# Optimization experiments

Hardware: AMD Instinct MI355X
Metric: run time of the kernel (lower is better)

The kernel has to match this reference:

```python
import jax, jax.numpy as jnp
import numpy as np

B, S, H = 4, 2048, 1024
NH, HD = 16, 64
LN_EPS = 1e-5


def _l2norm(x, axis=-1, eps=1e-12):
    n = jnp.sqrt(jnp.sum(x * x, axis=axis, keepdims=True))
    return x / jnp.maximum(n, eps)


def setup_inputs() -> dict:
    key = jax.random.key(0)
    ks = jax.random.split(key, 10)
    sd = 0.02
    x = jax.random.normal(ks[0], (B, S, H), jnp.float32)
    Wq = jax.random.normal(ks[1], (H, H), jnp.float32) * sd
    Wk = jax.random.normal(ks[2], (H, H), jnp.float32) * sd
    Wv = jax.random.normal(ks[3], (H, H), jnp.float32) * sd
    Wa = jax.random.normal(ks[4], (NH, H), jnp.float32) * sd
    ba = jnp.zeros((NH,), jnp.float32)
    Wb = jax.random.normal(ks[5], (NH, H), jnp.float32) * sd
    bb = jnp.zeros((NH,), jnp.float32)
    Wg = jax.random.normal(ks[6], (H, H), jnp.float32) * sd
    Wo = jax.random.normal(ks[7], (H, H), jnp.float32) * sd
    ln_g = jnp.ones((H,), jnp.float32)
    ln_b = jnp.zeros((H,), jnp.float32)
    return {"x": x, "Wq": Wq, "Wk": Wk, "Wv": Wv, "Wa": Wa, "ba": ba,
            "Wb": Wb, "bb": bb, "Wg": Wg, "Wo": Wo, "ln_g": ln_g, "ln_b": ln_b}


def _forward(x, Wq, Wk, Wv, Wa, ba, Wb, bb, Wg, Wo, ln_g, ln_b):
    q = _l2norm((x @ Wq.T).reshape(B, S, NH, HD))  # [B,S,nh,hd]
    k = _l2norm((x @ Wk.T).reshape(B, S, NH, HD))
    v = jax.nn.silu(x @ Wv.T).reshape(B, S, NH, HD)
    alpha = jax.nn.sigmoid(x @ Wa.T + ba)  # [B,S,nh]
    beta = jax.nn.sigmoid(x @ Wb.T + bb)   # [B,S,nh]

    def step(state, inp):
        a_t, b_t, k_t, v_t, q_t = inp  # a,b: [B,nh]; k,v,q: [B,nh,hd]
        a_ = a_t[:, :, None, None]
        b_ = b_t[:, :, None, None]
        kk = k_t[..., :, None] * k_t[..., None, :]  # [B,nh,hd,hd]
        state = a_ * state * (1.0 - b_ * kk) + b_ * (v_t[..., :, None] * k_t[..., None, :])
        out_t = jnp.sum(state * q_t[..., None, :], axis=-1)  # [B,nh,hd]
        return state, out_t

    # time-major xs for scan
    xs = (jnp.moveaxis(alpha, 1, 0), jnp.moveaxis(beta, 1, 0),
          jnp.moveaxis(k, 1, 0), jnp.moveaxis(v, 1, 0), jnp.moveaxis(q, 1, 0))
    state0 = jnp.zeros((B, NH, HD, HD), x.dtype)
    _, outs = jax.lax.scan(step, state0, xs)  # [S,B,nh,hd]
    out = jnp.moveaxis(outs, 0, 1).reshape(B, S, H)

    # LayerNorm over total_dim
    mu = jnp.mean(out, axis=-1, keepdims=True)
    var = jnp.var(out, axis=-1, keepdims=True)
    out = (out - mu) / jnp.sqrt(var + LN_EPS) * ln_g + ln_b

    out = out * jax.nn.silu(x @ Wg.T)
    return out @ Wo.T


def reference(x, Wq, Wk, Wv, Wa, ba, Wb, bb, Wg, Wo, ln_g, ln_b):
    return _forward(x, Wq, Wk, Wv, Wa, ba, Wb, bb, Wg, Wo, ln_g, ln_b)
```

## Files before the change

### kernel.cpp

```cpp
#include <hip/hip_runtime.h>

typedef unsigned short u16;
typedef __bf16 bf16x8 __attribute__((ext_vector_type(8)));
typedef float f32x4 __attribute__((ext_vector_type(4)));

constexpr int Bq  = 4;
constexpr int Sq  = 2048;
constexpr int Hq  = 1024;
constexpr int NHq = 16;
constexpr int HDq = 64;
constexpr int CCH = 16;
constexpr int LCH = 128;

constexpr size_t OFF_WB = 0;
constexpr size_t OFF_XB = 10485760;
constexpr size_t OFF_Q  = 27262976;
constexpr size_t OFF_K  = 60817408;
constexpr size_t OFF_V  = 94371840;
constexpr size_t OFF_G  = 127926272;
constexpr size_t OFF_AL = 161480704;
constexpr size_t OFF_BE = 162004992;
constexpr size_t OFF_P  = 162529280;
constexpr size_t OFF_O  = 179306496;

__device__ __forceinline__ u16 f2bf(float f) {
  unsigned u = __float_as_uint(f);
  u += 0x7fffu + ((u >> 16) & 1u);
  return (u16)(u >> 16);
}
__device__ __forceinline__ float sigmoidf_(float x) { return 1.f / (1.f + __expf(-x)); }

__device__ __forceinline__ void async16(const void* g, void* l) {
  __builtin_amdgcn_global_load_lds((const __attribute__((address_space(1))) void*)g,
                                   (__attribute__((address_space(3))) void*)l, 16, 0, 0);
}

__global__ __launch_bounds__(256) void cvt_x_kernel(const float* __restrict__ in, u16* __restrict__ outp) {
  const size_t i = ((size_t)blockIdx.x * 256 + threadIdx.x) * 4;
  float4 f = *(const float4*)(in + i);
  ushort4 u; u.x = f2bf(f.x); u.y = f2bf(f.y); u.z = f2bf(f.z); u.w = f2bf(f.w);
  *(ushort4*)(outp + i) = u;
}

__global__ __launch_bounds__(256) void cvt_w_kernel(const float* __restrict__ w0, const float* __restrict__ w1,
    const float* __restrict__ w2, const float* __restrict__ w3, const float* __restrict__ w4,
    u16* __restrict__ outp) {
  const int z = blockIdx.z;
  const float* src = (z == 0) ? w0 : (z == 1) ? w1 : (z == 2) ? w2 : (z == 3) ? w3 : w4;
  const size_t i = ((size_t)blockIdx.x * 256 + threadIdx.x) * 4;
  float4 f = *(const float4*)(src + i);
  ushort4 u; u.x = f2bf(f.x); u.y = f2bf(f.y); u.z = f2bf(f.z); u.w = f2bf(f.w);
  *(ushort4*)(outp + (size_t)z * (1024 * 1024) + i) = u;
}

__global__ __launch_bounds__(256) void cvt_ab_kernel(const float* __restrict__ Wa, const float* __restrict__ Wb,
    u16* __restrict__ outp) {
  const size_t i = ((size_t)blockIdx.x * 256 + threadIdx.x) * 4;
  const int row = (int)(i >> 10);
  ushort4 u;
  if (row < 32) {
    const float* src = (row < 16) ? (Wa + i) : (Wb + i - 16 * 1024);
    float4 f = *(const float4*)src;
    u.x = f2bf(f.x); u.y = f2bf(f.y); u.z = f2bf(f.z); u.w = f2bf(f.w);
  } else {
    u.x = u.y = u.z = u.w = 0;
  }
  *(ushort4*)(outp + i) = u;
}

__global__ __launch_bounds__(256) void gemm_bt(const u16* __restrict__ A, const u16* __restrict__ Wall,
    const u16* __restrict__ Wab,
    float* __restrict__ Cq, float* __restrict__ Ck, float* __restrict__ Cv, float* __restrict__ Cg,
    float* __restrict__ al, float* __restrict__ be,
    const float* __restrict__ ba, const float* __restrict__ bb, int mode) {
  constexpr int GK = 1024, GN = 1024;
  const int z = blockIdx.z;
  if (mode == 1 && z == 4 && blockIdx.y > 0) return;
  __shared__ __align__(16) u16 As[128 * 32];
  __shared__ __align__(16) u16 Bs[128 * 32];
  const int tid = threadIdx.x;
  const int w = tid >> 6, lane = tid & 63;
  const int m0 = blockIdx.x * 128, n0 = blockIdx.y * 128;
  const u16* W = (mode == 1 && z == 4) ? Wab : (Wall + (size_t)z * (1024 * 1024));
  const int rrow = lane >> 2;
  const int kc8 = (lane & 3) * 8;
  const u16* gA = A + (size_t)(m0 + w * 32 + rrow) * GK + kc8;
  const u16* gB = W + (size_t)(n0 + w * 32 + rrow) * GK + kc8;
  u16* lA = As + (w * 32) * 32;
  u16* lB = Bs + (w * 32) * 32;
  const int qd = lane >> 4, l15 = lane & 15;
  const int wm = (w >> 1) * 64, wn = (w & 1) * 64;
  f32x4 acc[4][4] = {};
  for (int kt = 0; kt < GK; kt += 32) {
    async16(gA,           lA);
    async16(gA + 16 * GK, lA + 16 * 32);
    async16(gB,           lB);
    async16(gB + 16 * GK, lB + 16 * 32);
    gA += 32; gB += 32;
    __syncthreads();
    bf16x8 af[4], bfr[4];
    #pragma unroll
    for (int i = 0; i < 4; ++i) {
      af[i]  = *(const bf16x8*)(As + (wm + i * 16 + l15) * 32 + qd * 8);
      bfr[i] = *(const bf16x8*)(Bs + (wn + i * 16 + l15) * 32 + qd * 8);
    }
    #pragma unroll
    for (int i = 0; i < 4; ++i)
      #pragma unroll
      for (int j = 0; j < 4; ++j)
        acc[i][j] = __builtin_amdgcn_mfma_f32_16x16x32_bf16(af[i], bfr[j], acc[i][j], 0, 0, 0);
    __syncthreads();
  }
  if (mode == 1 && z == 4) {
    if (wn == 0) {
      const float bav = ba[l15], bbv = bb[l15];
      #pragma unroll
      for (int i = 0; i < 4; ++i) {
        const int row = m0 + wm + i * 16 + qd * 4;
        #pragma unroll
        for (int r = 0; r < 4; ++r) {
          al[(size_t)(row + r) * 16 + l15] = sigmoidf_(acc[i][0][r] + bav);
          be[(size_t)(row + r) * 16 + l15] = sigmoidf_(acc[i][1][r] + bbv);
        }
      }
    }
    return;
  }
  if (mode == 1 && (z == 0 || z == 1)) {
    #pragma unroll
    for (int i = 0; i < 4; ++i)
      #pragma unroll
      for (int r = 0; r < 4; ++r) {
        float ss = acc[i][0][r] * acc[i][0][r] + acc[i][1][r] * acc[i][1][r]
                 + acc[i][2][r] * acc[i][2][r] + acc[i][3][r] * acc[i][3][r];
        ss += __shfl_xor(ss, 1); ss += __shfl_xor(ss, 2);
        ss += __shfl_xor(ss, 4); ss += __shfl_xor(ss, 8);
        const float rn = 1.f / fmaxf(sqrtf(ss), 1e-12f);
        acc[i][0][r] *= rn; acc[i][1][r] *= rn; acc[i][2][r] *= rn; acc[i][3][r] *= rn;
      }
  } else if (mode == 1 && z == 2) {
    #pragma unroll
    for (int i = 0; i < 4; ++i)
      #pragma unroll
      for (int j = 0; j < 4; ++j)
        #pragma unroll
        for (int r = 0; r < 4; ++r)
          acc[i][j][r] = acc[i][j][r] * sigmoidf_(acc[i][j][r]);
  }
  float* C = (mode == 0) ? Cq : ((z == 0) ? Cq : (z == 1) ? Ck : (z == 2) ? Cv : Cg);
  #pragma unroll
  for (int i = 0; i < 4; ++i) {
    const int row = m0 + wm + i * 16 + qd * 4;
    #pragma unroll
    for (int j = 0; j < 4; ++j) {
      const int col = n0 + wn + j * 16 + l15;
      #pragma unroll
      for (int r = 0; r < 4; ++r)
        C[(size_t)(row + r) * GN + col] = acc[i][j][r];
    }
  }
}

struct ScanLds1 { float kb[2][4][16 * 64]; float vb[2][4][16 * 64]; float ab[2][4][32]; };
struct ScanLds2 { float kb[2][4][16 * 64]; float qb[2][4][16 * 64]; float vb[2][4][16 * 64]; float ab[2][4][32]; };

__global__ __launch_bounds__(256) void scan_p1(const float* __restrict__ k, const float* __restrict__ v,
    const float* __restrict__ al, const float* __restrict__ be,
    float* __restrict__ P, float* __restrict__ Q) {
  __shared__ ScanLds1 L;
  const int tid = threadIdx.x, wv = tid >> 6, lane = tid & 63;
  const int bh = blockIdx.x >> 2;
  const int c = (blockIdx.x & 3) * 4 + wv;
  const int b = bh >> 4, h = bh & 15;
  const int r8 = (lane >> 3) * 8, c8 = (lane & 7) * 8;
  const size_t base0 = ((size_t)(b * Sq + c * LCH)) * 1024 + h * 64;
  const size_t ab0   = ((size_t)(b * Sq + c * LCH)) * 16 + h;
  const int tokw = lane >> 4, seg = lane & 15;
  auto stage = [&](int tile, int bi) {
    const size_t tb = base0 + (size_t)tile * 16 * 1024;
    #pragma unroll
    for (int i = 0; i < 4; ++i) {
      async16(k + tb + (size_t)(i * 4 + tokw) * 1024 + seg * 4, &L.kb[bi][wv][i * 256]);
      async16(v + tb + (size_t)(i * 4 + tokw) * 1024 + seg * 4, &L.vb[bi][wv][i * 256]);
    }
    if (lane < 32) {
      const float* src = (lane < 16) ? al : be;
      const int tt = lane & 15;
      L.ab[bi][wv][(lane < 16 ? 0 : 16) + tt] = src[ab0 + (size_t)(tile * 16 + tt) * 16];
    }
  };
  float Pr[64], Qr[64];
  #pragma unroll
  for (int i = 0; i < 64; ++i) { Pr[i] = 1.f; Qr[i] = 0.f; }
  stage(0, 0);
  for (int tile = 0; tile < 8; ++tile) {
    __syncthreads();
    if (tile < 7) stage(tile + 1, (tile + 1) & 1);
    const int bi = tile & 1;
    const float* kbp = L.kb[bi][wv];
    const float* vbp = L.vb[bi][wv];
    const float* abp = L.ab[bi][wv];
    #pragma unroll 2
    for (int tt = 0; tt < 16; ++tt) {
      const float a = abp[tt], bt = abp[16 + tt];
      float4 kcv0 = *(const float4*)(kbp + tt * 64 + c8);
      float4 kcv1 = *(const float4*)(kbp + tt * 64 + c8 + 4);
      float4 krv0 = *(const float4*)(kbp + tt * 64 + r8);
      float4 krv1 = *(const float4*)(kbp + tt * 64 + r8 + 4);
      float4 vrv0 = *(const float4*)(vbp + tt * 64 + r8);
      float4 vrv1 = *(const float4*)(vbp + tt * 64 + r8 + 4);
      const float kcv[8] = {kcv0.x, kcv0.y, kcv0.z, kcv0.w, kcv1.x, kcv1.y, kcv1.z, kcv1.w};
      const float krv[8] = {krv0.x, krv0.y, krv0.z, krv0.w, krv1.x, krv1.y, krv1.z, krv1.w};
      const float vrv[8] = {vrv0.x, vrv0.y, vrv0.z, vrv0.w, vrv1.x, vrv1.y, vrv1.z, vrv1.w};
      const float abt = a * bt;
      float c1[8], c2[8];
      #pragma unroll
      for (int i = 0; i < 8; ++i) { c1[i] = abt * krv[i]; c2[i] = bt * vrv[i]; }
      #pragma unroll
      for (int i = 0; i < 8; ++i)
        #pragma unroll
        for (int j = 0; j < 8; ++j) {
          const int e = i * 8 + j;
          const float A = fmaf(-c1[i], kcv[j], a);
          Qr[e] = fmaf(A, Qr[e], c2[i] * kcv[j]);
          Pr[e] *= A;
        }
    }
  }
  const size_t pbase = ((size_t)bh * CCH + c) * 4096 + (size_t)c8;
  #pragma unroll
  for (int i = 0; i < 8; ++i) {
    const size_t pi = pbase + (size_t)(r8 + i) * 64;
    *(float4*)(P + pi)     = make_float4(Pr[i*8],   Pr[i*8+1], Pr[i*8+2], Pr[i*8+3]);
    *(float4*)(P + pi + 4) = make_float4(Pr[i*8+4], Pr[i*8+5], Pr[i*8+6], Pr[i*8+7]);
    *(float4*)(Q + pi)     = make_float4(Qr[i*8],   Qr[i*8+1], Qr[i*8+2], Qr[i*8+3]);
    *(float4*)(Q + pi + 4) = make_float4(Qr[i*8+4], Qr[i*8+5], Qr[i*8+6], Qr[i*8+7]);
  }
}

__global__ __launch_bounds__(256) void scan_comb(float* __restrict__ P, const float* __restrict__ Q) {
  const int g = blockIdx.x * 256 + threadIdx.x;
  const int elem = g & 4095;
  const int bh = g >> 12;
  float s = 0.f;
  for (int c = 0; c < CCH; ++c) {
    const size_t idx = ((size_t)bh * CCH + c) * 4096 + elem;
    const float p = P[idx], qq = Q[idx];
    P[idx] = s;
    s = fmaf(p, s, qq);
  }
}

__global__ __launch_bounds__(256) void scan_p2(const float* __restrict__ q, const float* __restrict__ k,
    const float* __restrict__ v, const float* __restrict__ al, const float* __restrict__ be,
    const float* __restrict__ Pini, float* __restrict__ o) {
  __shared__ ScanLds2 L;
  const int tid = threadIdx.x, wv = tid >> 6, lane = tid & 63;
  const int bh = blockIdx.x >> 2;
  const int c = (blockIdx.x & 3) * 4 + wv;
  const int b = bh >> 4, h = bh & 15;
  const int cb = lane & 7;
  const int r8 = (lane >> 3) * 8, c8 = cb * 8;
  const size_t base0 = ((size_t)(b * Sq + c * LCH)) * 1024 + h * 64;
  const size_t ab0   = ((size_t)(b * Sq + c * LCH)) * 16 + h;
  const size_t pbase = ((size_t)bh * CCH + c) * 4096 + (size_t)c8;
  const int tokw = lane >> 4, seg = lane & 15;
  auto stage = [&](int tile, int bi) {
    const size_t tb = base0 + (size_t)tile * 16 * 1024;
    #pragma unroll
    for (int i = 0; i < 4; ++i) {
      async16(k + tb + (size_t)(i * 4 + tokw) * 1024 + seg * 4, &L.kb[bi][wv][i * 256]);
      async16(q + tb + (size_t)(i * 4 + tokw) * 1024 + seg * 4, &L.qb[bi][wv][i * 256]);
      async16(v + tb + (size_t)(i * 4 + tokw) * 1024 + seg * 4, &L.vb[bi][wv][i * 256]);
    }
    if (lane < 32) {
      const float* src = (lane < 16) ? al : be;
      const int tt = lane & 15;
      L.ab[bi][wv][(lane < 16 ? 0 : 16) + tt] = src[ab0 + (size_t)(tile * 16 + tt) * 16];
    }
  };
  float st[64];
  #pragma unroll
  for (int i = 0; i < 8; ++i) {
    float4 s0 = *(const float4*)(Pini + pbase + (size_t)(r8 + i) * 64);
    float4 s1 = *(const float4*)(Pini + pbase + (size_t)(r8 + i) * 64 + 4);
    st[i*8]   = s0.x; st[i*8+1] = s0.y; st[i*8+2] = s0.z; st[i*8+3] = s0.w;
    st[i*8+4] = s1.x; st[i*8+5] = s1.y; st[i*8+6] = s1.z; st[i*8+7] = s1.w;
  }
  stage(0, 0);
  const bool hi4 = (cb & 4), hi2 = (cb & 2), hi1 = (cb & 1);
  for (int tile = 0; tile < 8; ++tile) {
    __syncthreads();
    if (tile < 7) stage(tile + 1, (tile + 1) & 1);
    const int bi = tile & 1;
    const float* kbp = L.kb[bi][wv];
    const float* qbp = L.qb[bi][wv];
    const float* vbp = L.vb[bi][wv];
    const float* abp = L.ab[bi][wv];
    #pragma unroll 2
    for (int tt = 0; tt < 16; ++tt) {
      const int t = tile * 16 + tt;
      const float a = abp[tt], bt = abp[16 + tt];
      float4 kcv0 = *(const float4*)(kbp + tt * 64 + c8);
      float4 kcv1 = *(const float4*)(kbp + tt * 64 + c8 + 4);
      float4 qcv0 = *(const float4*)(qbp + tt * 64 + c8);
      float4 qcv1 = *(const float4*)(qbp + tt * 64 + c8 + 4);
      float4 krv0 = *(const float4*)(kbp + tt * 64 + r8);
      float4 krv1 = *(const float4*)(kbp + tt * 64 + r8 + 4);
      float4 vrv0 = *(const float4*)(vbp + tt * 64 + r8);
      float4 vrv1 = *(const float4*)(vbp + tt * 64 + r8 + 4);
      const float kcv[8] = {kcv0.x, kcv0.y, kcv0.z, kcv0.w, kcv1.x, kcv1.y, kcv1.z, kcv1.w};
      const float qcv[8] = {qcv0.x, qcv0.y, qcv0.z, qcv0.w, qcv1.x, qcv1.y, qcv1.z, qcv1.w};
      const float krv[8] = {krv0.x, krv0.y, krv0.z, krv0.w, krv1.x, krv1.y, krv1.z, krv1.w};
      const float vrv[8] = {vrv0.x, vrv0.y, vrv0.z, vrv0.w, vrv1.x, vrv1.y, vrv1.z, vrv1.w};
      const float abt = a * bt;
      float c1[8], c2[8];
      #pragma unroll
      for (int i = 0; i < 8; ++i) { c1[i] = abt * krv[i]; c2[i] = bt * vrv[i]; }
      float p[8];
      #pragma unroll
      for (int i = 0; i < 8; ++i) p[i] = 0.f;
      #pragma unroll
      for (int i = 0; i < 8; ++i)
        #pragma unroll
        for (int j = 0; j < 8; ++j) {
          const int e = i * 8 + j;
          const float A = fmaf(-c1[i], kcv[j], a);
          st[e] = fmaf(A, st[e], c2[i] * kcv[j]);
          p[i] = fmaf(st[e], qcv[j], p[i]);
        }
      float r4[4];
      #pragma unroll
      for (int i = 0; i < 4; ++i) {
        const float send = hi4 ? p[i] : p[i + 4];
        const float recv = __shfl_xor(send, 4);
        r4[i] = (hi4 ? p[i + 4] : p[i]) + recv;
      }
      float r2[2];
      #pragma unroll
      for (int i = 0; i < 2; ++i) {
        const float send = hi2 ? r4[i] : r4[i + 2];
        const float recv = __shfl_xor(send, 2);
        r2[i] = (hi2 ? r4[i + 2] : r4[i]) + recv;
      }
      {
        const float send = hi1 ? r2[0] : r2[1];
        const float recv = __shfl_xor(send, 1);
        const float tot = (hi1 ? r2[1] : r2[0]) + recv;
        o[base0 + (size_t)t * 1024 + lane] = tot;
      }
    }
  }
}

__global__ __launch_bounds__(256) void ln_gate_kernel(const float* __restrict__ o, const float* __restrict__ g,
    const float* __restrict__ ln_g, const float* __restrict__ ln_b, u16* __restrict__ y) {
  const int t = blockIdx.x, tid = threadIdx.x;
  const size_t row = (size_t)t * 1024;
  float4 xv = *(const float4*)(o + row + tid * 4);
  float s  = xv.x + xv.y + xv.z + xv.w;
  float s2 = xv.x * xv.x + xv.y * xv.y + xv.z * xv.z + xv.w * xv.w;
  #pragma unroll
  for (int m = 1; m < 64; m <<= 1) { s += __shfl_xor(s, m); s2 += __shfl_xor(s2, m); }
  __shared__ float red[8];
  const int w = tid >> 6, lane = tid & 63;
  if (lane == 0) { red[w] = s; red[4 + w] = s2; }
  __syncthreads();
  s  = red[0] + red[1] + red[2] + red[3];
  s2 = red[4] + red[5] + red[6] + red[7];
  const float mu = s * (1.f / 1024.f);
  const float var = s2 * (1.f / 1024.f) - mu * mu;
  const float rstd = rsqrtf(var + 1e-5f);
  float4 gv = *(const float4*)(g + row + tid * 4);
  float4 lg = *(const float4*)(ln_g + tid * 4);
  float4 lb = *(const float4*)(ln_b + tid * 4);
  ushort4 u;
  u.x = f2bf(((xv.x - mu) * rstd * lg.x + lb.x) * (gv.x * sigmoidf_(gv.x)));
  u.y = f2bf(((xv.y - mu) * rstd * lg.y + lb.y) * (gv.y * sigmoidf_(gv.y)));
  u.z = f2bf(((xv.z - mu) * rstd * lg.z + lb.z) * (gv.z * sigmoidf_(gv.z)));
  u.w = f2bf(((xv.w - mu) * rstd * lg.w + lb.w) * (gv.w * sigmoidf_(gv.w)));
  *(ushort4*)(y + row + tid * 4) = u;
}

extern "C" void kernel_launch(void* const* d_in, const int* in_sizes, int n_in,
                              void* d_out, int out_size, void* d_ws, size_t ws_size,
                              hipStream_t stream) {
  const float* x    = (const float*)d_in[0];
  const float* Wq   = (const float*)d_in[1];
  const float* Wk   = (const float*)d_in[2];
  const float* Wv   = (const float*)d_in[3];
  const float* Wa   = (const float*)d_in[4];
  const float* ba   = (const float*)d_in[5];
  const float* Wb   = (const float*)d_in[6];
  const float* bb   = (const float*)d_in[7];
  const float* Wg   = (const float*)d_in[8];
  const float* Wo   = (const float*)d_in[9];
  const float* ln_g = (const float*)d_in[10];
  const float* ln_b = (const float*)d_in[11];
  float* out = (float*)d_out;
  char* ws = (char*)d_ws;

  u16*   wb  = (u16*)(ws + OFF_WB);
  u16*   xb  = (u16*)(ws + OFF_XB);
  float* qf  = (float*)(ws + OFF_Q);
  float* kf  = (float*)(ws + OFF_K);
  float* vf  = (float*)(ws + OFF_V);
  float* gf  = (float*)(ws + OFF_G);
  float* al  = (float*)(ws + OFF_AL);
  float* be  = (float*)(ws + OFF_BE);
  u16*   wab = (u16*)(ws + OFF_P);
  float* Pb  = (float*)(ws + OFF_P);
  float* Qc  = (float*)(ws + OFF_XB);
  float* of  = (float*)(ws + OFF_O);
  u16*   yb  = xb;

  cvt_x_kernel<<<8192, 256, 0, stream>>>(x, xb);
  cvt_w_kernel<<<dim3(1024, 1, 5), 256, 0, stream>>>(Wq, Wk, Wv, Wg, Wo, wb);
  cvt_ab_kernel<<<128, 256, 0, stream>>>(Wa, Wb, wab);
  gemm_bt<<<dim3(64, 8, 5), 256, 0, stream>>>(xb, wb, wab, qf, kf, vf, gf, al, be, ba, bb, 1);
  scan_p1<<<256, 256, 0, stream>>>(kf, vf, al, be, Pb, Qc);
  scan_comb<<<1024, 256, 0, stream>>>(Pb, Qc);
  scan_p2<<<256, 256, 0, stream>>>(qf, kf, vf, al, be, Pb, of);
  ln_gate_kernel<<<8192, 256, 0, stream>>>(of, gf, ln_g, ln_b, yb);
  gemm_bt<<<dim3(64, 8, 1), 256, 0, stream>>>(yb, wb + (size_t)4 * 1024 * 1024, wab,
                                              out, out, out, out, al, be, ba, bb, 0);
}
```

Measured before the change: 454.6 us.

## Split each scan chunk's state rows across two waves to double scan parallelism

Both chunked scan passes now give each 64x64 state chunk to two waves, each owning 32 rows (4x8 per lane), instead of one wave per chunk. Each block covers two chunks and the grid grows from 256 to 512 blocks, with launch bounds asking for two blocks per CU. The aim is to halve per-thread register state and double the wave count, so the scan's latency-bound inner loop gets more occupancy on 256 CUs. Staging work is redistributed across all four waves, and the output reduction drops one shuffle level but half the lanes now sit idle on stores.

Measured after the change: 447.8 us. Within noise of the previous version (-1.5%).

```diff
diff --git a/kernel.cpp b/kernel.cpp
--- a/kernel.cpp
+++ b/kernel.cpp
@@ -161,63 +161,67 @@
   }
 }
 
-struct ScanLds1 { float kb[2][4][16 * 64]; float vb[2][4][16 * 64]; float ab[2][4][32]; };
-struct ScanLds2 { float kb[2][4][16 * 64]; float qb[2][4][16 * 64]; float vb[2][4][16 * 64]; float ab[2][4][32]; };
-
-__global__ __launch_bounds__(256) void scan_p1(const float* __restrict__ k, const float* __restrict__ v,
+struct ScanLds1 { float kb[2][2][16 * 64]; float vb[2][2][16 * 64]; float ab[2][2][32]; };
+struct ScanLds2 { float kb[2][2][16 * 64]; float qb[2][2][16 * 64]; float vb[2][2][16 * 64]; float ab[2][2][32]; };
+
+__global__ __launch_bounds__(256, 2) void scan_p1(const float* __restrict__ k, const float* __restrict__ v,
     const float* __restrict__ al, const float* __restrict__ be,
     float* __restrict__ P, float* __restrict__ Q) {
   __shared__ ScanLds1 L;
   const int tid = threadIdx.x, wv = tid >> 6, lane = tid & 63;
-  const int bh = blockIdx.x >> 2;
-  const int c = (blockIdx.x & 3) * 4 + wv;
+  const int bh = blockIdx.x >> 3, cp = blockIdx.x & 7;
   const int b = bh >> 4, h = bh & 15;
-  const int r8 = (lane >> 3) * 8, c8 = (lane & 7) * 8;
-  const size_t base0 = ((size_t)(b * Sq + c * LCH)) * 1024 + h * 64;
-  const size_t ab0   = ((size_t)(b * Sq + c * LCH)) * 16 + h;
+  const int cw = wv >> 1, half = wv & 1;
+  const int c = cp * 2 + cw;
+  const int rg = lane >> 3, cg = lane & 7;
+  const int r0 = half * 32 + rg * 4, c8 = cg * 8;
+  const size_t base0[2] = { ((size_t)(b * Sq + (cp * 2 + 0) * LCH)) * 1024 + h * 64,
+                            ((size_t)(b * Sq + (cp * 2 + 1) * LCH)) * 1024 + h * 64 };
+  const size_t ab0[2]   = { ((size_t)(b * Sq + (cp * 2 + 0) * LCH)) * 16 + h,
+                            ((size_t)(b * Sq + (cp * 2 + 1) * LCH)) * 16 + h };
   const int tokw = lane >> 4, seg = lane & 15;
   auto stage = [&](int tile, int bi) {
-    const size_t tb = base0 + (size_t)tile * 16 * 1024;
-    #pragma unroll
-    for (int i = 0; i < 4; ++i) {
-      async16(k + tb + (size_t)(i * 4 + tokw) * 1024 + seg * 4, &L.kb[bi][wv][i * 256]);
-      async16(v + tb + (size_t)(i * 4 + tokw) * 1024 + seg * 4, &L.vb[bi][wv][i * 256]);
-    }
-    if (lane < 32) {
-      const float* src = (lane < 16) ? al : be;
-      const int tt = lane & 15;
-      L.ab[bi][wv][(lane < 16 ? 0 : 16) + tt] = src[ab0 + (size_t)(tile * 16 + tt) * 16];
+    #pragma unroll
+    for (int j = 0; j < 4; ++j) {
+      const int job = wv * 4 + j;
+      const int ch = job >> 3, rem = job & 7, arr = rem >> 2, i = rem & 3;
+      const float* src = arr ? v : k;
+      float* dst = arr ? &L.vb[bi][ch][i * 256] : &L.kb[bi][ch][i * 256];
+      async16(src + base0[ch] + (size_t)(tile * 16 + i * 4 + tokw) * 1024 + seg * 4, dst);
+    }
+    if (wv == 0) {
+      const int ch = lane >> 5, w16 = (lane >> 4) & 1, tt = lane & 15;
+      const float* s = w16 ? be : al;
+      L.ab[bi][ch][w16 * 16 + tt] = s[ab0[ch] + (size_t)(tile * 16 + tt) * 16];
     }
   };
-  float Pr[64], Qr[64];
+  float Pr[32], Qr[32];
   #pragma unroll
-  for (int i = 0; i < 64; ++i) { Pr[i] = 1.f; Qr[i] = 0.f; }
+  for (int i = 0; i < 32; ++i) { Pr[i] = 1.f; Qr[i] = 0.f; }
   stage(0, 0);
   for (int tile = 0; tile < 8; ++tile) {
     __syncthreads();
     if (tile < 7) stage(tile + 1, (tile + 1) & 1);
     const int bi = tile & 1;
-    const float* kbp = L.kb[bi][wv];
-    const float* vbp = L.vb[bi][wv];
-    const float* abp = L.ab[bi][wv];
+    const float* kbp = L.kb[bi][cw];
+    const float* vbp = L.vb[bi][cw];
+    const float* abp = L.ab[bi][cw];
     #pragma unroll 2
     for (int tt = 0; tt < 16; ++tt) {
       const float a = abp[tt], bt = abp[16 + tt];
       float4 kcv0 = *(const float4*)(kbp + tt * 64 + c8);
       float4 kcv1 = *(const float4*)(kbp + tt * 64 + c8 + 4);
-      float4 krv0 = *(const float4*)(kbp + tt * 64 + r8);
-      float4 krv1 = *(const float4*)(kbp + tt * 64 + r8 + 4);
-      float4 vrv0 = *(const float4*)(vbp + tt * 64 + r8);
-      float4 vrv1 = *(const float4*)(vbp + tt * 64 + r8 + 4);
+      float4 krvv = *(const float4*)(kbp + tt * 64 + r0);
+      float4 vrvv = *(const float4*)(vbp + tt * 64 + r0);
       const float kcv[8] = {kcv0.x, kcv0.y, kcv0.z, kcv0.w, kcv1.x, kcv1.y, kcv1.z, kcv1.w};
-      const float krv[8] = {krv0.x, krv0.y, krv0.z, krv0.w, krv1.x, krv1.y, krv1.z, krv1.w};
-      const float vrv[8] = {vrv0.x, vrv0.y, vrv0.z, vrv0.w, vrv1.x, vrv1.y, vrv1.z, vrv1.w};
+      const float krv[4] = {krvv.x, krvv.y, krvv.z, krvv.w};
+      const float vrv[4] = {vrvv.x, vrvv.y, vrvv.z, vrvv.w};
       const float abt = a * bt;
-      float c1[8], c2[8];
-      #pragma unroll
-      for (int i = 0; i < 8; ++i) { c1[i] = abt * krv[i]; c2[i] = bt * vrv[i]; }
-      #pragma unroll
-      for (int i = 0; i < 8; ++i)
+      float c1[4], c2[4];
+      #pragma unroll
+      for (int i = 0; i < 4; ++i) { c1[i] = abt * krv[i]; c2[i] = bt * vrv[i]; }
+      #pragma unroll
+      for (int i = 0; i < 4; ++i)
         #pragma unroll
         for (int j = 0; j < 8; ++j) {
           const int e = i * 8 + j;
@@ -229,11 +233,11 @@
   }
   const size_t pbase = ((size_t)bh * CCH + c) * 4096 + (size_t)c8;
   #pragma unroll
-  for (int i = 0; i < 8; ++i) {
-    const size_t pi = pbase + (size_t)(r8 + i) * 64;
-    *(float4*)(P + pi)     = make_float4(Pr[i*8],   Pr[i*8+1], Pr[i*8+2], Pr[i*8+3]);
+  for (int i = 0; i < 4; ++i) {
+    const size_t pi = pbase + (size_t)(r0 + i) * 64;
+    *(float4*)(P + pi) = make_float4(Pr[i*8],   Pr[i*8+1], Pr[i*8+2], Pr[i*8+3]);
     *(float4*)(P + pi + 4) = make_float4(Pr[i*8+4], Pr[i*8+5], Pr[i*8+6], Pr[i*8+7]);
-    *(float4*)(Q + pi)     = make_float4(Qr[i*8],   Qr[i*8+1], Qr[i*8+2], Qr[i*8+3]);
+    *(float4*)(Q + pi) = make_float4(Qr[i*8],   Qr[i*8+1], Qr[i*8+2], Qr[i*8+3]);
     *(float4*)(Q + pi + 4) = make_float4(Qr[i*8+4], Qr[i*8+5], Qr[i*8+6], Qr[i*8+7]);
   }
 }
@@ -251,52 +255,60 @@
   }
 }
 
-__global__ __launch_bounds__(256) void scan_p2(const float* __restrict__ q, const float* __restrict__ k,
+__global__ __launch_bounds__(256, 2) void scan_p2(const float* __restrict__ q, const float* __restrict__ k,
     const float* __restrict__ v, const float* __restrict__ al, const float* __restrict__ be,
     const float* __restrict__ Pini, float* __restrict__ o) {
   __shared__ ScanLds2 L;
   const int tid = threadIdx.x, wv = tid >> 6, lane = tid & 63;
-  const int bh = blockIdx.x >> 2;
-  const int c = (blockIdx.x & 3) * 4 + wv;
+  const int bh = blockIdx.x >> 3, cp = blockIdx.x & 7;
   const int b = bh >> 4, h = bh & 15;
-  const int cb = lane & 7;
-  const int r8 = (lane >> 3) * 8, c8 = cb * 8;
-  const size_t base0 = ((size_t)(b * Sq + c * LCH)) * 1024 + h * 64;
-  const size_t ab0   = ((size_t)(b * Sq + c * LCH)) * 16 + h;
+  const int cw = wv >> 1, half = wv & 1;
+  const int c = cp * 2 + cw;
+  const int rg = lane >> 3, cg = lane & 7;
+  const int r0 = half * 32 + rg * 4, c8 = cg * 8;
+  const size_t base0[2] = { ((size_t)(b * Sq + (cp * 2 + 0) * LCH)) * 1024 + h * 64,
+                            ((size_t)(b * Sq + (cp * 2 + 1) * LCH)) * 1024 + h * 64 };
+  const size_t ab0[2]   = { ((size_t)(b * Sq + (cp * 2 + 0) * LCH)) * 16 + h,
+                            ((size_t)(b * Sq + (cp * 2 + 1) * LCH)) * 16 + h };
+  const size_t mybase = base0[cw];
   const size_t pbase = ((size_t)bh * CCH + c) * 4096 + (size_t)c8;
   const int tokw = lane >> 4, seg = lane & 15;
   auto stage = [&](int tile, int bi) {
-    const size_t tb = base0 + (size_t)tile * 16 * 1024;
-    #pragma unroll
-    for (int i = 0; i < 4; ++i) {
-      async16(k + tb + (size_t)(i * 4 + tokw) * 1024 + seg * 4, &L.kb[bi][wv][i * 256]);
-      async16(q + tb + (size_t)(i * 4 + tokw) * 1024 + seg * 4, &L.qb[bi][wv][i * 256]);
-      async16(v + tb + (size_t)(i * 4 + tokw) * 1024 + seg * 4, &L.vb[bi][wv][i * 256]);
-    }
-    if (lane < 32) {
-      const float* src = (lane < 16) ? al : be;
-      const int tt = lane & 15;
-      L.ab[bi][wv][(lane < 16 ? 0 : 16) + tt] = src[ab0 + (size_t)(tile * 16 + tt) * 16];
+    #pragma unroll
+    for (int j = 0; j < 6; ++j) {
+      const int job = wv * 6 + j;
+      const int ch = job / 12, rem = job % 12, arr = rem >> 2, i = rem & 3;
+      const float* src = (arr == 0) ? k : (arr == 1) ? q : v;
+      float* dst = (arr == 0) ? &L.kb[bi][ch][i * 256] : (arr == 1) ? &L.qb[bi][ch][i * 256]
+                                                                    : &L.vb[bi][ch][i * 256];
+      async16(src + base0[ch] + (size_t)(tile * 16 + i * 4 + tokw) * 1024 + seg * 4, dst);
+    }
+    if (wv == 0) {
+      const int ch = lane >> 5, w16 = (lane >> 4) & 1, tt = lane & 15;
+      const float* s = w16 ? be : al;
+      L.ab[bi][ch][w16 * 16 + tt] = s[ab0[ch] + (size_t)(tile * 16 + tt) * 16];
     }
   };
-  float st[64];
+  float st[32];
   #pragma unroll
-  for (int i = 0; i < 8; ++i) {
-    float4 s0 = *(const float4*)(Pini + pbase + (size_t)(r8 + i) * 64);
-    float4 s1 = *(const float4*)(Pini + pbase + (size_t)(r8 + i) * 64 + 4);
+  for (int i = 0; i < 4; ++i) {
+    float4 s0 = *(const float4*)(Pini + pbase + (size_t)(r0 + i) * 64);
+    float4 s1 = *(const float4*)(Pini + pbase + (size_t)(r0 + i) * 64 + 4);
     st[i*8]   = s0.x; st[i*8+1] = s0.y; st[i*8+2] = s0.z; st[i*8+3] = s0.w;
     st[i*8+4] = s1.x; st[i*8+5] = s1.y; st[i*8+6] = s1.z; st[i*8+7] = s1.w;
   }
   stage(0, 0);
-  const bool hi4 = (cb & 4), hi2 = (cb & 2), hi1 = (cb & 1);
+  const bool hi4 = (cg & 4), hi2 = (cg & 2);
+  const int rowIdx = r0 + (cg >> 1);
+  const bool doStore = ((cg & 1) == 0);
   for (int tile = 0; tile < 8; ++tile) {
     __syncthreads();
     if (tile < 7) stage(tile + 1, (tile + 1) & 1);
     const int bi = tile & 1;
-    const float* kbp = L.kb[bi][wv];
-    const float* qbp = L.qb[bi][wv];
-    const float* vbp = L.vb[bi][wv];
-    const float* abp = L.ab[bi][wv];
+    const float* kbp = L.kb[bi][cw];
+    const float* qbp = L.qb[bi][cw];
+    const float* vbp = L.vb[bi][cw];
+    const float* abp = L.ab[bi][cw];
     #pragma unroll 2
     for (int tt = 0; tt < 16; ++tt) {
       const int t = tile * 16 + tt;
@@ -305,23 +317,21 @@
       float4 kcv1 = *(const float4*)(kbp + tt * 64 + c8 + 4);
       float4 qcv0 = *(const float4*)(qbp + tt * 64 + c8);
       float4 qcv1 = *(const float4*)(qbp + tt * 64 + c8 + 4);
-      float4 krv0 = *(const float4*)(kbp + tt * 64 + r8);
-      float4 krv1 = *(const float4*)(kbp + tt * 64 + r8 + 4);
-      float4 vrv0 = *(const float4*)(vbp + tt * 64 + r8);
-      float4 vrv1 = *(const float4*)(vbp + tt * 64 + r8 + 4);
+      float4 krvv = *(const float4*)(kbp + tt * 64 + r0);
+      float4 vrvv = *(const float4*)(vbp + tt * 64 + r0);
       const float kcv[8] = {kcv0.x, kcv0.y, kcv0.z, kcv0.w, kcv1.x, kcv1.y, kcv1.z, kcv1.w};
       const float qcv[8] = {qcv0.x, qcv0.y, qcv0.z, qcv0.w, qcv1.x, qcv1.y, qcv1.z, qcv1.w};
-      const float krv[8] = {krv0.x, krv0.y, krv0.z, krv0.w, krv1.x, krv1.y, krv1.z, krv1.w};
-      const float vrv[8] = {vrv0.x, vrv0.y, vrv0.z, vrv0.w, vrv1.x, vrv1.y, vrv1.z, vrv1.w};
+      const float krv[4] = {krvv.x, krvv.y, krvv.z, krvv.w};
+      const float vrv[4] = {vrvv.x, vrvv.y, vrvv.z, vrvv.w};
       const float abt = a * bt;
-      float c1[8], c2[8];
-      #pragma unroll
-      for (int i = 0; i < 8; ++i) { c1[i] = abt * krv[i]; c2[i] = bt * vrv[i]; }
-      float p[8];
-      #pragma unroll
-      for (int i = 0; i < 8; ++i) p[i] = 0.f;
-      #pragma unroll
-      for (int i = 0; i < 8; ++i)
+      float c1[4], c2[4];
+      #pragma unroll
+      for (int i = 0; i < 4; ++i) { c1[i] = abt * krv[i]; c2[i] = bt * vrv[i]; }
+      float p[4];
+      #pragma unroll
+      for (int i = 0; i < 4; ++i) p[i] = 0.f;
+      #pragma unroll
+      for (int i = 0; i < 4; ++i)
         #pragma unroll
         for (int j = 0; j < 8; ++j) {
           const int e = i * 8 + j;
@@ -329,26 +339,21 @@
           st[e] = fmaf(A, st[e], c2[i] * kcv[j]);
           p[i] = fmaf(st[e], qcv[j], p[i]);
         }
-      float r4[4];
-      #pragma unroll
-      for (int i = 0; i < 4; ++i) {
-        const float send = hi4 ? p[i] : p[i + 4];
+      float r2[2];
+      #pragma unroll
+      for (int i = 0; i < 2; ++i) {
+        const float send = hi4 ? p[i] : p[i + 2];
         const float recv = __shfl_xor(send, 4);
-        r4[i] = (hi4 ? p[i + 4] : p[i]) + recv;
+        r2[i] = (hi4 ? p[i + 2] : p[i]) + recv;
       }
-      float r2[2];
-      #pragma unroll
-      for (int i = 0; i < 2; ++i) {
-        const float send = hi2 ? r4[i] : r4[i + 2];
+      float r1;
+      {
+        const float send = hi2 ? r2[0] : r2[1];
         const float recv = __shfl_xor(send, 2);
-        r2[i] = (hi2 ? r4[i + 2] : r4[i]) + recv;
+        r1 = (hi2 ? r2[1] : r2[0]) + recv;
       }
-      {
-        const float send = hi1 ? r2[0] : r2[1];
-        const float recv = __shfl_xor(send, 1);
-        const float tot = (hi1 ? r2[1] : r2[0]) + recv;
-        o[base0 + (size_t)t * 1024 + lane] = tot;
-      }
+      const float tot = r1 + __shfl_xor(r1, 1);
+      if (doStore) o[mybase + (size_t)t * 1024 + rowIdx] = tot;
     }
   }
 }
@@ -418,9 +423,9 @@
   cvt_w_kernel<<<dim3(1024, 1, 5), 256, 0, stream>>>(Wq, Wk, Wv, Wg, Wo, wb);
   cvt_ab_kernel<<<128, 256, 0, stream>>>(Wa, Wb, wab);
   gemm_bt<<<dim3(64, 8, 5), 256, 0, stream>>>(xb, wb, wab, qf, kf, vf, gf, al, be, ba, bb, 1);
-  scan_p1<<<256, 256, 0, stream>>>(kf, vf, al, be, Pb, Qc);
+  scan_p1<<<512, 256, 0, stream>>>(kf, vf, al, be, Pb, Qc);
   scan_comb<<<1024, 256, 0, stream>>>(Pb, Qc);
-  scan_p2<<<256, 256, 0, stream>>>(qf, kf, vf, al, be, Pb, of);
+  scan_p2<<<512, 256, 0, stream>>>(qf, kf, vf, al, be, Pb, of);
   ln_gate_kernel<<<8192, 256, 0, stream>>>(of, gf, ln_g, ln_b, yb);
   gemm_bt<<<dim3(64, 8, 1), 256, 0, stream>>>(yb, wb + (size_t)4 * 1024 * 1024, wab,
                                               out, out, out, out, al, be, ba, bb, 0);
```
